# Performance work log

Measured on AMD Instinct MI355X. Metric: run time of the kernel, lower is better.

## Reference

```python
import jax, jax.numpy as jnp
import numpy as np

VOCAB = 100000
EMB = 256
HID = 512
HDIR = HID // 2
T = 10            # tagset size
START = 8
STOP = 9
S = 4096          # sequence length
NEG = -10000.0


def setup_inputs() -> dict:
    key = jax.random.key(0)
    ks = jax.random.split(key, 16)
    sentence = jax.random.randint(ks[0], (S,), 0, VOCAB)
    emb = jax.random.normal(ks[1], (VOCAB, EMB), dtype=jnp.float32) * 0.02
    s = 1.0 / np.sqrt(HDIR).astype(np.float32)

    def lstm_weights(k):
        k1, k2, k3, k4 = jax.random.split(k, 4)
        return (
            jax.random.uniform(k1, (4 * HDIR, EMB), jnp.float32, -s, s),
            jax.random.uniform(k2, (4 * HDIR, HDIR), jnp.float32, -s, s),
            jax.random.uniform(k3, (4 * HDIR,), jnp.float32, -s, s),
            jax.random.uniform(k4, (4 * HDIR,), jnp.float32, -s, s),
        )

    Wih_f, Whh_f, bih_f, bhh_f = lstm_weights(ks[2])
    Wih_b, Whh_b, bih_b, bhh_b = lstm_weights(ks[3])
    so = 1.0 / np.sqrt(HID).astype(np.float32)
    W_out = jax.random.uniform(ks[4], (T, HID), jnp.float32, -so, so)
    b_out = jax.random.uniform(ks[5], (T,), jnp.float32, -so, so)
    transitions = jax.random.normal(ks[6], (T, T), dtype=jnp.float32)
    transitions = transitions.at[START, :].set(NEG).at[:, STOP].set(NEG)
    return {
        "sentence": sentence, "emb": emb,
        "Wih_f": Wih_f, "Whh_f": Whh_f, "bih_f": bih_f, "bhh_f": bhh_f,
        "Wih_b": Wih_b, "Whh_b": Whh_b, "bih_b": bih_b, "bhh_b": bhh_b,
        "W_out": W_out, "b_out": b_out, "transitions": transitions,
    }


def _lstm_dir(x, Wih, Whh, bih, bhh):
    # x: [S, EMB] -> hidden states [S, HDIR]; PyTorch gate order i,f,g,o
    b = bih + bhh
    xW = x @ Wih.T + b  # precompute input contribution: [S, 4*HDIR]

    def step(carry, xw_t):
        h, c = carry
        z = xw_t + Whh @ h
        i, f, g, o = jnp.split(z, 4)
        i = jax.nn.sigmoid(i); f = jax.nn.sigmoid(f)
        g = jnp.tanh(g); o = jax.nn.sigmoid(o)
        c = f * c + i * g
        h = o * jnp.tanh(c)
        return (h, c), h

    h0 = jnp.zeros((HDIR,), x.dtype)
    _, hs = jax.lax.scan(step, (h0, h0), xW)
    return hs


def _viterbi(feats, transitions):
    # feats: [S, T]
    def vstep(fv, feat):
        ntv = fv[None, :] + transitions        # [T(next), T(prev)]
        bp = jnp.argmax(ntv, axis=1)           # [T]
        fv_new = jnp.max(ntv, axis=1) + feat   # [T]
        return fv_new, bp

    init = jnp.full((T,), NEG, feats.dtype).at[START].set(0.0)
    fv, bps = jax.lax.scan(vstep, init, feats)
    terminal = fv + transitions[STOP]
    best = jnp.argmax(terminal)
    score = terminal[best]

    def back(tag, bp):
        return bp[tag], tag

    _, path_rev = jax.lax.scan(back, best, bps[::-1])
    return score, path_rev[::-1]


def reference(sentence, emb, Wih_f, Whh_f, bih_f, bhh_f,
              Wih_b, Whh_b, bih_b, bhh_b, W_out, b_out, transitions):
    x = emb[sentence]                                   # [S, EMB]
    h_f = _lstm_dir(x, Wih_f, Whh_f, bih_f, bhh_f)      # [S, HDIR]
    h_b = _lstm_dir(x[::-1], Wih_b, Whh_b, bih_b, bhh_b)[::-1]
    lstm_out = jnp.concatenate([h_f, h_b], axis=-1)     # [S, HID]
    feats = lstm_out @ W_out.T + b_out                  # [S, T]
    score, path = _viterbi(feats, transitions)
    return score, path
```

## Files before the change

### kernel.cpp

```cpp
#include <hip/hip_runtime.h>
#include <math.h>

#define S_LEN 4096
#define HDIRC 256
#define NTAG 10
#define START_TAG 8
#define STOP_TAG 9
#define NEGV -10000.0f

#define XW_OFF 0UL
#define XW_SZ  (2UL * S_LEN * 1024)
#define HS_OFF (XW_OFF + XW_SZ)
#define HS_SZ  (2UL * S_LEN * 256)
#define WT_OFF (HS_OFF + HS_SZ)
#define WT_SZ  (2UL * 256 * 1024)
#define FE_OFF (WT_OFF + WT_SZ)
#define FE_SZ  ((size_t)S_LEN * NTAG)
#define RING_OFF (FE_OFF + FE_SZ)
#define RING_SZ (2UL * 2 * 256 * 2)

__global__ void transpose_wih(const float* __restrict__ wf,
                              const float* __restrict__ wb,
                              float* __restrict__ wT) {
    __shared__ float tile[32][33];
    const float* src = blockIdx.z ? wb : wf;
    float* dst = wT + (size_t)blockIdx.z * 256 * 1024;
    int x = blockIdx.x * 32 + threadIdx.x;
    int y = blockIdx.y * 32 + threadIdx.y;
    tile[threadIdx.y][threadIdx.x] = src[y * 256 + x];
    __syncthreads();
    int ko = blockIdx.x * 32 + threadIdx.y;
    int ro = blockIdx.y * 32 + threadIdx.x;
    dst[(size_t)ko * 1024 + ro] = tile[threadIdx.x][threadIdx.y];
}

__global__ __launch_bounds__(256) void xw_gemm(
    const int* __restrict__ sent, const float* __restrict__ emb,
    const float* __restrict__ wT,
    const float* __restrict__ bih_f, const float* __restrict__ bhh_f,
    const float* __restrict__ bih_b, const float* __restrict__ bhh_b,
    float* __restrict__ xw) {
    int dir = blockIdx.y;
    int t0 = blockIdx.x * 16;
    int tid = threadIdx.x;
    __shared__ __align__(16) float xs[16][256];
    for (int i = 0; i < 16; ++i) {
        int t = t0 + i;
        int pos = dir ? (S_LEN - 1 - t) : t;
        int idx = sent[pos];
        xs[i][tid] = emb[(size_t)idx * 256 + tid];
    }
    __syncthreads();
    const float* w = wT + (size_t)dir * 256 * 1024;
    const float* bi = dir ? bih_b : bih_f;
    const float* bh = dir ? bhh_b : bhh_f;
    float4 bv;
    bv.x = bi[4 * tid + 0] + bh[4 * tid + 0];
    bv.y = bi[4 * tid + 1] + bh[4 * tid + 1];
    bv.z = bi[4 * tid + 2] + bh[4 * tid + 2];
    bv.w = bi[4 * tid + 3] + bh[4 * tid + 3];
    float4 acc[16];
#pragma unroll
    for (int i = 0; i < 16; ++i) acc[i] = bv;
    for (int k4 = 0; k4 < 64; ++k4) {
        float4 w0 = ((const float4*)(w + (size_t)(4 * k4 + 0) * 1024))[tid];
        float4 w1 = ((const float4*)(w + (size_t)(4 * k4 + 1) * 1024))[tid];
        float4 w2 = ((const float4*)(w + (size_t)(4 * k4 + 2) * 1024))[tid];
        float4 w3 = ((const float4*)(w + (size_t)(4 * k4 + 3) * 1024))[tid];
#pragma unroll
        for (int i = 0; i < 16; ++i) {
            float4 xv = *(const float4*)&xs[i][4 * k4];
            acc[i].x = fmaf(w0.x, xv.x, acc[i].x);
            acc[i].y = fmaf(w0.y, xv.x, acc[i].y);
            acc[i].z = fmaf(w0.z, xv.x, acc[i].z);
            acc[i].w = fmaf(w0.w, xv.x, acc[i].w);
            acc[i].x = fmaf(w1.x, xv.y, acc[i].x);
            acc[i].y = fmaf(w1.y, xv.y, acc[i].y);
            acc[i].z = fmaf(w1.z, xv.y, acc[i].z);
            acc[i].w = fmaf(w1.w, xv.y, acc[i].w);
            acc[i].x = fmaf(w2.x, xv.z, acc[i].x);
            acc[i].y = fmaf(w2.y, xv.z, acc[i].y);
            acc[i].z = fmaf(w2.z, xv.z, acc[i].z);
            acc[i].w = fmaf(w2.w, xv.z, acc[i].w);
            acc[i].x = fmaf(w3.x, xv.w, acc[i].x);
            acc[i].y = fmaf(w3.y, xv.w, acc[i].y);
            acc[i].z = fmaf(w3.z, xv.w, acc[i].z);
            acc[i].w = fmaf(w3.w, xv.w, acc[i].w);
        }
    }
#pragma unroll
    for (int i = 0; i < 16; ++i)
        ((float4*)(xw + ((size_t)dir * S_LEN + t0 + i) * 1024))[tid] = acc[i];
}

__global__ __launch_bounds__(256, 1) void lstm_rec(
    const float* __restrict__ whh_f, const float* __restrict__ whh_b,
    const float* __restrict__ xw, float* __restrict__ hs,
    unsigned long long* __restrict__ ring) {
    int blk = blockIdx.x;
    int dir = blk >> 4;
    int b = blk & 15;
    int tid = threadIdx.x;
    int g = tid >> 6;
    int lane = tid & 63;
    int v = lane >> 2;
    int u = lane & 3;

    __shared__ __align__(16) float wl[16384];
    __shared__ __align__(16) float hbf[320];
    __shared__ __align__(16) float zp2[1280];
    float4* wl4 = (float4*)wl;

    const float* whh = dir ? whh_b : whh_f;
#pragma unroll
    for (int j = 0; j < 4; ++j)
#pragma unroll
        for (int i = 0; i < 4; ++i)
            wl4[((g * 16 + j * 4 + i) << 6) + lane] =
                *(const float4*)(whh +
                    (size_t)(g * 256 + b * 16 + 4 * u + j) * 256 + 16 * v + 4 * i);

    const float* xwd = xw + (size_t)dir * S_LEN * 1024;
    float* hsd = hs + (size_t)dir * S_LEN * 256;
    unsigned long long* ringd = ring + dir * 512;

    for (int i = tid; i < 320; i += 256) hbf[i] = 0.f;
    float c = 0.f;
    int crow = (lane >> 4) * 256 + b * 16 + (lane & 15);
    float xw_cur = (g == 0) ? xwd[crow] : 0.f;
    __syncthreads();

    for (int t = 0; t < S_LEN; ++t) {
        const float4* hb4 = (const float4*)hbf + v * 5;
        float4 hc[4];
#pragma unroll
        for (int i = 0; i < 4; ++i) hc[i] = hb4[i];
        float4 acc[4];
#pragma unroll
        for (int j = 0; j < 4; ++j) acc[j] = make_float4(0.f, 0.f, 0.f, 0.f);
#pragma unroll
        for (int j = 0; j < 4; ++j) {
#pragma unroll
            for (int i = 0; i < 4; ++i) {
                float4 wv = wl4[((g * 16 + j * 4 + i) << 6) + lane];
                acc[j].x = fmaf(wv.x, hc[i].x, acc[j].x);
                acc[j].y = fmaf(wv.y, hc[i].y, acc[j].y);
                acc[j].z = fmaf(wv.z, hc[i].z, acc[j].z);
                acc[j].w = fmaf(wv.w, hc[i].w, acc[j].w);
            }
        }
#pragma unroll
        for (int j = 0; j < 4; ++j)
            zp2[(g * 16 + 4 * u + j) * 20 + v] =
                (acc[j].x + acc[j].y) + (acc[j].z + acc[j].w);
        __syncthreads();

        if (g == 0) {
            const float4* zrow = (const float4*)&zp2[lane * 20];
            float4 z0 = zrow[0], z1 = zrow[1], z2 = zrow[2], z3 = zrow[3];
            float z = xw_cur +
                (((z0.x + z0.y) + (z0.z + z0.w)) + ((z1.x + z1.y) + (z1.z + z1.w))) +
                (((z2.x + z2.y) + (z2.z + z2.w)) + ((z3.x + z3.y) + (z3.z + z3.w)));
            int g2 = lane >> 4;
            int tn = (t + 1 < S_LEN) ? t + 1 : t;
            float xw_next = xwd[(size_t)tn * 1024 + crow];
            float act = (g2 == 2) ? tanhf(z) : 1.f / (1.f + expf(-z));
            float fg = __shfl(act, (lane & 15) + 16, 64);
            float gg = __shfl(act, (lane & 15) + 32, 64);
            float og = __shfl(act, (lane & 15) + 48, 64);
            unsigned long long* slot = ringd + (size_t)(t & 1) * 256;
            unsigned int want = (unsigned int)(t + 1);
            if (lane < 16) {
                c = fmaf(fg, c, act * gg);
                float h = og * tanhf(c);
                hsd[(size_t)t * 256 + b * 16 + lane] = h;
                unsigned long long pk = ((unsigned long long)want << 32) |
                                        (unsigned long long)__float_as_uint(h);
                __hip_atomic_store(&slot[b * 16 + lane], pk,
                                   __ATOMIC_RELAXED, __HIP_MEMORY_SCOPE_AGENT);
            }
            unsigned long long v0, v1, v2, v3;
            for (;;) {
                v0 = __hip_atomic_load(&slot[lane], __ATOMIC_RELAXED, __HIP_MEMORY_SCOPE_AGENT);
                v1 = __hip_atomic_load(&slot[lane + 64], __ATOMIC_RELAXED, __HIP_MEMORY_SCOPE_AGENT);
                v2 = __hip_atomic_load(&slot[lane + 128], __ATOMIC_RELAXED, __HIP_MEMORY_SCOPE_AGENT);
                v3 = __hip_atomic_load(&slot[lane + 192], __ATOMIC_RELAXED, __HIP_MEMORY_SCOPE_AGENT);
                bool ok = ((unsigned int)(v0 >> 32) == want) &
                          ((unsigned int)(v1 >> 32) == want) &
                          ((unsigned int)(v2 >> 32) == want) &
                          ((unsigned int)(v3 >> 32) == want);
                if (__all(ok)) break;
            }
            int sl = lane & 15, ch = lane >> 4;
            hbf[(ch + 0) * 20 + sl]  = __uint_as_float((unsigned int)v0);
            hbf[(ch + 4) * 20 + sl]  = __uint_as_float((unsigned int)v1);
            hbf[(ch + 8) * 20 + sl]  = __uint_as_float((unsigned int)v2);
            hbf[(ch + 12) * 20 + sl] = __uint_as_float((unsigned int)v3);
            xw_cur = xw_next;
        }
        __syncthreads();
    }
}

__global__ __launch_bounds__(64) void feats_k(const float* __restrict__ hs,
                                              const float* __restrict__ wout,
                                              const float* __restrict__ bout,
                                              float* __restrict__ feats) {
    int t = blockIdx.x, tau = blockIdx.y, lane = threadIdx.x;
    const float* hf = hs + (size_t)t * 256;
    const float* hbk = hs + (size_t)S_LEN * 256 + (size_t)(S_LEN - 1 - t) * 256;
    const float* w = wout + (size_t)tau * 512;
    float s = 0.f;
#pragma unroll
    for (int m = 0; m < 4; ++m) s = fmaf(w[lane + 64 * m], hf[lane + 64 * m], s);
#pragma unroll
    for (int m = 0; m < 4; ++m) s = fmaf(w[256 + lane + 64 * m], hbk[lane + 64 * m], s);
#pragma unroll
    for (int off = 32; off > 0; off >>= 1) s += __shfl_down(s, off, 64);
    if (lane == 0) feats[(size_t)t * NTAG + tau] = s + bout[tau];
}

__global__ __launch_bounds__(64) void viterbi_k(const float* __restrict__ feats,
                                                const float* __restrict__ trans,
                                                float* __restrict__ out) {
    __shared__ float fstage[128 * NTAG];
    __shared__ unsigned char bp[S_LEN * NTAG];
    __shared__ float path[S_LEN];
    __shared__ float fvbuf[NTAG];
    __shared__ float term[NTAG];
    int tid = threadIdx.x;
    float tr[NTAG];
    float trstop = 0.f;
    if (tid < NTAG) {
#pragma unroll
        for (int j = 0; j < NTAG; ++j) tr[j] = trans[tid * NTAG + j];
        trstop = trans[STOP_TAG * NTAG + tid];
    }
    float fv = (tid == START_TAG) ? 0.f : NEGV;
    for (int t0 = 0; t0 < S_LEN; t0 += 128) {
        __syncthreads();
        for (int i = tid; i < 128 * NTAG; i += 64) fstage[i] = feats[(size_t)t0 * NTAG + i];
        __syncthreads();
        for (int tt = 0; tt < 128; ++tt) {
            int t = t0 + tt;
            if (tid < NTAG) fvbuf[tid] = fv;
            __syncthreads();
            if (tid < NTAG) {
                float best = -3.4e38f; int bj = 0;
#pragma unroll
                for (int j = 0; j < NTAG; ++j) {
                    float v = fvbuf[j] + tr[j];
                    if (v > best) { best = v; bj = j; }
                }
                bp[t * NTAG + tid] = (unsigned char)bj;
                fv = best + fstage[tt * NTAG + tid];
            }
            __syncthreads();
        }
    }
    if (tid < NTAG) term[tid] = fv + trstop;
    __syncthreads();
    if (tid == 0) {
        float best = -3.4e38f; int bi = 0;
#pragma unroll
        for (int i = 0; i < NTAG; ++i) {
            float v = term[i];
            if (v > best) { best = v; bi = i; }
        }
        out[0] = best;
        int tag = bi;
        for (int t = S_LEN - 1; t >= 0; --t) {
            path[t] = (float)tag;
            tag = bp[t * NTAG + tag];
        }
    }
    __syncthreads();
    for (int i = tid; i < S_LEN; i += 64) out[1 + i] = path[i];
}

extern "C" void kernel_launch(void* const* d_in, const int* in_sizes, int n_in,
                              void* d_out, int out_size, void* d_ws, size_t ws_size,
                              hipStream_t stream) {
    const int* sent = (const int*)d_in[0];
    const float* emb = (const float*)d_in[1];
    const float* wih_f = (const float*)d_in[2];
    const float* whh_f = (const float*)d_in[3];
    const float* bih_f = (const float*)d_in[4];
    const float* bhh_f = (const float*)d_in[5];
    const float* wih_b = (const float*)d_in[6];
    const float* whh_b = (const float*)d_in[7];
    const float* bih_b = (const float*)d_in[8];
    const float* bhh_b = (const float*)d_in[9];
    const float* wout = (const float*)d_in[10];
    const float* bout = (const float*)d_in[11];
    const float* trans = (const float*)d_in[12];

    float* ws = (float*)d_ws;
    float* xw = ws + XW_OFF;
    float* hs = ws + HS_OFF;
    float* wT = ws + WT_OFF;
    float* fe = ws + FE_OFF;
    unsigned long long* ring = (unsigned long long*)(ws + RING_OFF);

    hipLaunchKernelGGL(transpose_wih, dim3(8, 32, 2), dim3(32, 32), 0, stream,
                       wih_f, wih_b, wT);
    hipLaunchKernelGGL(xw_gemm, dim3(S_LEN / 16, 2), dim3(256), 0, stream,
                       sent, emb, wT, bih_f, bhh_f, bih_b, bhh_b, xw);
    hipLaunchKernelGGL(lstm_rec, dim3(32), dim3(256), 0, stream,
                       whh_f, whh_b, xw, hs, ring);
    hipLaunchKernelGGL(feats_k, dim3(S_LEN, NTAG), dim3(64), 0, stream,
                       hs, wout, bout, fe);
    hipLaunchKernelGGL(viterbi_k, dim3(1), dim3(64), 0, stream,
                       fe, trans, (float*)d_out);
}
```

Measured before the change: 8.177 ms.

## Keep LSTM recurrent weights in registers, reduce via shuffles, and use shuffle-based Viterbi

The LSTM recurrence now loads each thread's recurrent-weight slice into registers once, instead of re-reading it from LDS every step. Partial gate sums are reduced with cross-lane shuffles rather than through a shared staging buffer. Each warp applies the activation for its own gate, so the cell update reads four gate values from a small LDS buffer. The Viterbi kernel broadcasts the previous scores with shuffles inside its single wavefront and drops the two per-step barriers, and the input GEMM tile is halved to 8 timesteps to launch more blocks. Holding 64 floats of weights per thread raises register pressure, and relying on the wavefront running in lockstep in Viterbi is a correctness assumption.

After: 8.145 ms. No clear change (-0.4%).

```diff
diff --git a/kernel.cpp b/kernel.cpp
--- a/kernel.cpp
+++ b/kernel.cpp
@@ -41,10 +41,10 @@
     const float* __restrict__ bih_b, const float* __restrict__ bhh_b,
     float* __restrict__ xw) {
     int dir = blockIdx.y;
-    int t0 = blockIdx.x * 16;
+    int t0 = blockIdx.x * 8;
     int tid = threadIdx.x;
-    __shared__ __align__(16) float xs[16][256];
-    for (int i = 0; i < 16; ++i) {
+    __shared__ __align__(16) float xs[8][256];
+    for (int i = 0; i < 8; ++i) {
         int t = t0 + i;
         int pos = dir ? (S_LEN - 1 - t) : t;
         int idx = sent[pos];
@@ -59,16 +59,16 @@
     bv.y = bi[4 * tid + 1] + bh[4 * tid + 1];
     bv.z = bi[4 * tid + 2] + bh[4 * tid + 2];
     bv.w = bi[4 * tid + 3] + bh[4 * tid + 3];
-    float4 acc[16];
-#pragma unroll
-    for (int i = 0; i < 16; ++i) acc[i] = bv;
+    float4 acc[8];
+#pragma unroll
+    for (int i = 0; i < 8; ++i) acc[i] = bv;
     for (int k4 = 0; k4 < 64; ++k4) {
         float4 w0 = ((const float4*)(w + (size_t)(4 * k4 + 0) * 1024))[tid];
         float4 w1 = ((const float4*)(w + (size_t)(4 * k4 + 1) * 1024))[tid];
         float4 w2 = ((const float4*)(w + (size_t)(4 * k4 + 2) * 1024))[tid];
         float4 w3 = ((const float4*)(w + (size_t)(4 * k4 + 3) * 1024))[tid];
 #pragma unroll
-        for (int i = 0; i < 16; ++i) {
+        for (int i = 0; i < 8; ++i) {
             float4 xv = *(const float4*)&xs[i][4 * k4];
             acc[i].x = fmaf(w0.x, xv.x, acc[i].x);
             acc[i].y = fmaf(w0.y, xv.x, acc[i].y);
@@ -89,7 +89,7 @@
         }
     }
 #pragma unroll
-    for (int i = 0; i < 16; ++i)
+    for (int i = 0; i < 8; ++i)
         ((float4*)(xw + ((size_t)dir * S_LEN + t0 + i) * 1024))[tid] = acc[i];
 }
 
@@ -108,7 +108,7 @@
 
     __shared__ __align__(16) float wl[16384];
     __shared__ __align__(16) float hbf[320];
-    __shared__ __align__(16) float zp2[1280];
+    __shared__ __align__(16) float actb[64];
     float4* wl4 = (float4*)wl;
 
     const float* whh = dir ? whh_b : whh_f;
@@ -125,54 +125,102 @@
     unsigned long long* ringd = ring + dir * 512;
 
     for (int i = tid; i < 320; i += 256) hbf[i] = 0.f;
+    __syncthreads();
+
+    float4 w00 = wl4[((g * 16 + 0) << 6) + lane];
+    float4 w01 = wl4[((g * 16 + 1) << 6) + lane];
+    float4 w02 = wl4[((g * 16 + 2) << 6) + lane];
+    float4 w03 = wl4[((g * 16 + 3) << 6) + lane];
+    float4 w10 = wl4[((g * 16 + 4) << 6) + lane];
+    float4 w11 = wl4[((g * 16 + 5) << 6) + lane];
+    float4 w12 = wl4[((g * 16 + 6) << 6) + lane];
+    float4 w13 = wl4[((g * 16 + 7) << 6) + lane];
+    float4 w20 = wl4[((g * 16 + 8) << 6) + lane];
+    float4 w21 = wl4[((g * 16 + 9) << 6) + lane];
+    float4 w22 = wl4[((g * 16 + 10) << 6) + lane];
+    float4 w23 = wl4[((g * 16 + 11) << 6) + lane];
+    float4 w30 = wl4[((g * 16 + 12) << 6) + lane];
+    float4 w31 = wl4[((g * 16 + 13) << 6) + lane];
+    float4 w32 = wl4[((g * 16 + 14) << 6) + lane];
+    float4 w33 = wl4[((g * 16 + 15) << 6) + lane];
+
     float c = 0.f;
-    int crow = (lane >> 4) * 256 + b * 16 + (lane & 15);
-    float xw_cur = (g == 0) ? xwd[crow] : 0.f;
-    __syncthreads();
+    int crow = g * 256 + b * 16 + (lane & 15);
+    float xw_cur = (lane < 16) ? xwd[crow] : 0.f;
+    int sel = lane & 3;
 
     for (int t = 0; t < S_LEN; ++t) {
         const float4* hb4 = (const float4*)hbf + v * 5;
-        float4 hc[4];
-#pragma unroll
-        for (int i = 0; i < 4; ++i) hc[i] = hb4[i];
-        float4 acc[4];
-#pragma unroll
-        for (int j = 0; j < 4; ++j) acc[j] = make_float4(0.f, 0.f, 0.f, 0.f);
-#pragma unroll
-        for (int j = 0; j < 4; ++j) {
-#pragma unroll
-            for (int i = 0; i < 4; ++i) {
-                float4 wv = wl4[((g * 16 + j * 4 + i) << 6) + lane];
-                acc[j].x = fmaf(wv.x, hc[i].x, acc[j].x);
-                acc[j].y = fmaf(wv.y, hc[i].y, acc[j].y);
-                acc[j].z = fmaf(wv.z, hc[i].z, acc[j].z);
-                acc[j].w = fmaf(wv.w, hc[i].w, acc[j].w);
-            }
-        }
-#pragma unroll
-        for (int j = 0; j < 4; ++j)
-            zp2[(g * 16 + 4 * u + j) * 20 + v] =
-                (acc[j].x + acc[j].y) + (acc[j].z + acc[j].w);
+        float4 h0 = hb4[0], h1 = hb4[1], h2 = hb4[2], h3 = hb4[3];
+        float4 a0, a1, a2, a3;
+        a0.x = w00.x * h0.x; a0.y = w00.y * h0.y; a0.z = w00.z * h0.z; a0.w = w00.w * h0.w;
+        a1.x = w10.x * h0.x; a1.y = w10.y * h0.y; a1.z = w10.z * h0.z; a1.w = w10.w * h0.w;
+        a2.x = w20.x * h0.x; a2.y = w20.y * h0.y; a2.z = w20.z * h0.z; a2.w = w20.w * h0.w;
+        a3.x = w30.x * h0.x; a3.y = w30.y * h0.y; a3.z = w30.z * h0.z; a3.w = w30.w * h0.w;
+
+        a0.x = fmaf(w01.x, h1.x, a0.x); a0.y = fmaf(w01.y, h1.y, a0.y);
+        a0.z = fmaf(w01.z, h1.z, a0.z); a0.w = fmaf(w01.w, h1.w, a0.w);
+        a1.x = fmaf(w11.x, h1.x, a1.x); a1.y = fmaf(w11.y, h1.y, a1.y);
+        a1.z = fmaf(w11.z, h1.z, a1.z); a1.w = fmaf(w11.w, h1.w, a1.w);
+        a2.x = fmaf(w21.x, h1.x, a2.x); a2.y = fmaf(w21.y, h1.y, a2.y);
+        a2.z = fmaf(w21.z, h1.z, a2.z); a2.w = fmaf(w21.w, h1.w, a2.w);
+        a3.x = fmaf(w31.x, h1.x, a3.x); a3.y = fmaf(w31.y, h1.y, a3.y);
+        a3.z = fmaf(w31.z, h1.z, a3.z); a3.w = fmaf(w31.w, h1.w, a3.w);
+
+        a0.x = fmaf(w02.x, h2.x, a0.x); a0.y = fmaf(w02.y, h2.y, a0.y);
+        a0.z = fmaf(w02.z, h2.z, a0.z); a0.w = fmaf(w02.w, h2.w, a0.w);
+        a1.x = fmaf(w12.x, h2.x, a1.x); a1.y = fmaf(w12.y, h2.y, a1.y);
+        a1.z = fmaf(w12.z, h2.z, a1.z); a1.w = fmaf(w12.w, h2.w, a1.w);
+        a2.x = fmaf(w22.x, h2.x, a2.x); a2.y = fmaf(w22.y, h2.y, a2.y);
+        a2.z = fmaf(w22.z, h2.z, a2.z); a2.w = fmaf(w22.w, h2.w, a2.w);
+        a3.x = fmaf(w32.x, h2.x, a3.x); a3.y = fmaf(w32.y, h2.y, a3.y);
+        a3.z = fmaf(w32.z, h2.z, a3.z); a3.w = fmaf(w32.w, h2.w, a3.w);
+
+        a0.x = fmaf(w03.x, h3.x, a0.x); a0.y = fmaf(w03.y, h3.y, a0.y);
+        a0.z = fmaf(w03.z, h3.z, a0.z); a0.w = fmaf(w03.w, h3.w, a0.w);
+        a1.x = fmaf(w13.x, h3.x, a1.x); a1.y = fmaf(w13.y, h3.y, a1.y);
+        a1.z = fmaf(w13.z, h3.z, a1.z); a1.w = fmaf(w13.w, h3.w, a1.w);
+        a2.x = fmaf(w23.x, h3.x, a2.x); a2.y = fmaf(w23.y, h3.y, a2.y);
+        a2.z = fmaf(w23.z, h3.z, a2.z); a2.w = fmaf(w23.w, h3.w, a2.w);
+        a3.x = fmaf(w33.x, h3.x, a3.x); a3.y = fmaf(w33.y, h3.y, a3.y);
+        a3.z = fmaf(w33.z, h3.z, a3.z); a3.w = fmaf(w33.w, h3.w, a3.w);
+
+        float s0 = (a0.x + a0.y) + (a0.z + a0.w);
+        float s1 = (a1.x + a1.y) + (a1.z + a1.w);
+        float s2 = (a2.x + a2.y) + (a2.z + a2.w);
+        float s3 = (a3.x + a3.y) + (a3.z + a3.w);
+
+#pragma unroll
+        for (int off = 4; off < 64; off <<= 1) {
+            s0 += __shfl_xor(s0, off, 64);
+            s1 += __shfl_xor(s1, off, 64);
+            s2 += __shfl_xor(s2, off, 64);
+            s3 += __shfl_xor(s3, off, 64);
+        }
+        int srcl = lane >> 2;
+        float t0v = __shfl(s0, srcl, 64);
+        float t1v = __shfl(s1, srcl, 64);
+        float t2v = __shfl(s2, srcl, 64);
+        float t3v = __shfl(s3, srcl, 64);
+        float ss = (sel == 0) ? t0v : (sel == 1) ? t1v : (sel == 2) ? t2v : t3v;
+
+        int tn = (t + 1 < S_LEN) ? t + 1 : t;
+        float xw_next = 0.f;
+        if (lane < 16) {
+            float z = xw_cur + ss;
+            float act = (g == 2) ? tanhf(z) : 1.f / (1.f + expf(-z));
+            actb[(lane & 15) * 4 + g] = act;
+            xw_next = xwd[(size_t)tn * 1024 + crow];
+        }
         __syncthreads();
 
         if (g == 0) {
-            const float4* zrow = (const float4*)&zp2[lane * 20];
-            float4 z0 = zrow[0], z1 = zrow[1], z2 = zrow[2], z3 = zrow[3];
-            float z = xw_cur +
-                (((z0.x + z0.y) + (z0.z + z0.w)) + ((z1.x + z1.y) + (z1.z + z1.w))) +
-                (((z2.x + z2.y) + (z2.z + z2.w)) + ((z3.x + z3.y) + (z3.z + z3.w)));
-            int g2 = lane >> 4;
-            int tn = (t + 1 < S_LEN) ? t + 1 : t;
-            float xw_next = xwd[(size_t)tn * 1024 + crow];
-            float act = (g2 == 2) ? tanhf(z) : 1.f / (1.f + expf(-z));
-            float fg = __shfl(act, (lane & 15) + 16, 64);
-            float gg = __shfl(act, (lane & 15) + 32, 64);
-            float og = __shfl(act, (lane & 15) + 48, 64);
             unsigned long long* slot = ringd + (size_t)(t & 1) * 256;
             unsigned int want = (unsigned int)(t + 1);
             if (lane < 16) {
-                c = fmaf(fg, c, act * gg);
-                float h = og * tanhf(c);
+                float4 A = *(const float4*)&actb[lane * 4];
+                c = fmaf(A.y, c, A.x * A.z);
+                float h = A.w * tanhf(c);
                 hsd[(size_t)t * 256 + b * 16 + lane] = h;
                 unsigned long long pk = ((unsigned long long)want << 32) |
                                         (unsigned long long)__float_as_uint(h);
@@ -196,8 +244,8 @@
             hbf[(ch + 4) * 20 + sl]  = __uint_as_float((unsigned int)v1);
             hbf[(ch + 8) * 20 + sl]  = __uint_as_float((unsigned int)v2);
             hbf[(ch + 12) * 20 + sl] = __uint_as_float((unsigned int)v3);
-            xw_cur = xw_next;
-        }
+        }
+        xw_cur = xw_next;
         __syncthreads();
     }
 }
@@ -226,36 +274,40 @@
     __shared__ float fstage[128 * NTAG];
     __shared__ unsigned char bp[S_LEN * NTAG];
     __shared__ float path[S_LEN];
-    __shared__ float fvbuf[NTAG];
-    __shared__ float term[NTAG];
+    __shared__ float term[16];
     int tid = threadIdx.x;
+    int rr = (tid < NTAG) ? tid : 0;
     float tr[NTAG];
-    float trstop = 0.f;
-    if (tid < NTAG) {
-#pragma unroll
-        for (int j = 0; j < NTAG; ++j) tr[j] = trans[tid * NTAG + j];
-        trstop = trans[STOP_TAG * NTAG + tid];
-    }
+#pragma unroll
+    for (int j = 0; j < NTAG; ++j) tr[j] = trans[rr * NTAG + j];
+    float trstop = trans[STOP_TAG * NTAG + rr];
     float fv = (tid == START_TAG) ? 0.f : NEGV;
+
     for (int t0 = 0; t0 < S_LEN; t0 += 128) {
         __syncthreads();
         for (int i = tid; i < 128 * NTAG; i += 64) fstage[i] = feats[(size_t)t0 * NTAG + i];
         __syncthreads();
         for (int tt = 0; tt < 128; ++tt) {
-            int t = t0 + tt;
-            if (tid < NTAG) fvbuf[tid] = fv;
-            __syncthreads();
+            float b0 = __shfl(fv, 0, 64), b1 = __shfl(fv, 1, 64);
+            float b2 = __shfl(fv, 2, 64), b3 = __shfl(fv, 3, 64);
+            float b4 = __shfl(fv, 4, 64), b5 = __shfl(fv, 5, 64);
+            float b6 = __shfl(fv, 6, 64), b7 = __shfl(fv, 7, 64);
+            float b8 = __shfl(fv, 8, 64), b9 = __shfl(fv, 9, 64);
+            float best = b0 + tr[0]; int bj = 0;
+            float vv;
+            vv = b1 + tr[1]; if (vv > best) { best = vv; bj = 1; }
+            vv = b2 + tr[2]; if (vv > best) { best = vv; bj = 2; }
+            vv = b3 + tr[3]; if (vv > best) { best = vv; bj = 3; }
+            vv = b4 + tr[4]; if (vv > best) { best = vv; bj = 4; }
+            vv = b5 + tr[5]; if (vv > best) { best = vv; bj = 5; }
+            vv = b6 + tr[6]; if (vv > best) { best = vv; bj = 6; }
+            vv = b7 + tr[7]; if (vv > best) { best = vv; bj = 7; }
+            vv = b8 + tr[8]; if (vv > best) { best = vv; bj = 8; }
+            vv = b9 + tr[9]; if (vv > best) { best = vv; bj = 9; }
             if (tid < NTAG) {
-                float best = -3.4e38f; int bj = 0;
-#pragma unroll
-                for (int j = 0; j < NTAG; ++j) {
-                    float v = fvbuf[j] + tr[j];
-                    if (v > best) { best = v; bj = j; }
-                }
-                bp[t * NTAG + tid] = (unsigned char)bj;
+                bp[(t0 + tt) * NTAG + tid] = (unsigned char)bj;
                 fv = best + fstage[tt * NTAG + tid];
             }
-            __syncthreads();
         }
     }
     if (tid < NTAG) term[tid] = fv + trstop;
@@ -304,7 +356,7 @@
 
     hipLaunchKernelGGL(transpose_wih, dim3(8, 32, 2), dim3(32, 32), 0, stream,
                        wih_f, wih_b, wT);
-    hipLaunchKernelGGL(xw_gemm, dim3(S_LEN / 16, 2), dim3(256), 0, stream,
+    hipLaunchKernelGGL(xw_gemm, dim3(S_LEN / 8, 2), dim3(256), 0, stream,
                        sent, emb, wT, bih_f, bhh_f, bih_b, bhh_b, xw);
     hipLaunchKernelGGL(lstm_rec, dim3(32), dim3(256), 0, stream,
                        whh_f, whh_b, xw, hs, ring);
```
